# Kernel tuning notes

Hardware: AMD Instinct MI355X
Metric: run time of the kernel (lower is better)

Reference implementation:

```python
import jax, jax.numpy as jnp
import numpy as np

IN_DIM = 64
OUT_DIM = 128
GROUPS = 4
KS = 3
PAD = 1
SPLINE_ORDER = 3
GRID_SIZE = 5
GRID_K = GRID_SIZE + SPLINE_ORDER  # 8
GRID_LO, GRID_HI = -1.0, 1.0
_H = (GRID_HI - GRID_LO) / GRID_SIZE
GRID = jnp.linspace(GRID_LO - _H * SPLINE_ORDER, GRID_HI + _H * SPLINE_ORDER,
                    GRID_SIZE + 2 * SPLINE_ORDER + 1, dtype=jnp.float32)  # [14]
EPS = 1e-5


def _conv(x, w):
    # NCHW x OIHW -> NCHW, stride 1, dilation 1, padding PAD
    return jax.lax.conv_general_dilated(
        x, w, window_strides=(1, 1), padding=((PAD, PAD), (PAD, PAD)),
        dimension_numbers=('NCHW', 'OIHW', 'NCHW'))


def _bspline_bases(x):
    # Cox-de-Boor recursion; x: [B,C,H,W] -> [B, C*GRID_K, H, W]
    xu = x[..., None]  # [B,C,H,W,1]
    g = GRID
    bases = ((xu >= g[:-1]) & (xu < g[1:])).astype(x.dtype)  # [B,C,H,W,13]
    for k in range(1, SPLINE_ORDER + 1):
        left = g[:-(k + 1)]
        right = g[k:-1]
        delta = jnp.where(right == left, jnp.ones_like(right), right - left)
        bases = ((xu - left) / delta * bases[..., :-1]
                 + (g[k + 1:] - xu) / (g[k + 1:] - g[1:-k]) * bases[..., 1:])
    B, C, H, W, K = bases.shape  # K == GRID_K
    # moveaxis(-1, 2) then flatten(1, 2): channel-major, basis-minor ordering
    return jnp.moveaxis(bases, -1, 2).reshape(B, C * K, H, W)


def setup_inputs() -> dict:
    key = jax.random.key(0)
    k1, k2 = jax.random.split(key)
    x = jax.random.normal(k1, (8, IN_DIM, 64, 64), dtype=jnp.float32)
    # layer_weight: [out/g, (in/g)*(grid_k+1), ks, ks] = [32, 144, 3, 3]
    layer_weight = jax.random.normal(
        k2, (OUT_DIM // GROUPS, (IN_DIM // GROUPS) * (GRID_K + 1), KS, KS),
        dtype=jnp.float32) * 0.05
    prelu_w = jnp.full((GROUPS,), 0.25, dtype=jnp.float32)  # torch PReLU init
    return {"x": x, "layer_weight": layer_weight, "prelu_w": prelu_w}


def reference(x, layer_weight, prelu_w):
    cin_g = IN_DIM // GROUPS
    cout_g = OUT_DIM // GROUPS
    base_w = layer_weight[:, -cin_g:].reshape(cout_g, cin_g, KS, KS)
    spline_w = layer_weight[:, :-cin_g].reshape(cout_g, cin_g * GRID_K, KS, KS)
    outs = []
    for g in range(GROUPS):
        xg = x[:, g * cin_g:(g + 1) * cin_g]
        base_out = _conv(jax.nn.gelu(xg, approximate=False), base_w)
        spline_out = _conv(_bspline_bases(xg), spline_w)
        y = base_out + spline_out
        # InstanceNorm2d (affine=False): per-sample per-channel spatial norm
        mu = y.mean(axis=(2, 3), keepdims=True)
        var = y.var(axis=(2, 3), keepdims=True)
        y = (y - mu) / jnp.sqrt(var + EPS)
        # PReLU with scalar slope per group
        y = jnp.where(y >= 0, y, prelu_w[g] * y)
        outs.append(y)
    return jnp.concatenate(outs, axis=1)  # [B, OUT_DIM, H, W]
```

## Files before the change

### kernel.cpp

```cpp
#include <hip/hip_runtime.h>
#include <hip/hip_bf16.h>
#include <math.h>

typedef __attribute__((ext_vector_type(8))) short short8;
typedef __attribute__((ext_vector_type(4))) float f32x4;

__global__ void wtrans(const float* __restrict__ lw, ushort* __restrict__ w2) {
    int t = blockIdx.x * 256 + threadIdx.x;
    if (t >= 5760) return;
    int l    = t & 63;
    int page = t >> 6;
    int nt  = page & 1;
    int ks  = (page >> 1) % 5;
    int tap = page / 10;
    int oc = nt * 16 + (l & 15);
    int kbase = ks * 32 + (l >> 4) * 8;
    short8 v;
#pragma unroll
    for (int e = 0; e < 8; ++e) {
        int k = kbase + e;
        float val = (k < 144) ? lw[(oc * 144 + k) * 9 + tap] : 0.f;
        __hip_bfloat16 hb = __float2bfloat16(val);
        v[e] = *(short*)&hb;
    }
    ((short8*)w2)[t] = v;
}

__global__ __launch_bounds__(256) void kanconv(const float* __restrict__ x,
                                               const ushort* __restrict__ w2,
                                               float* __restrict__ y) {
    __shared__ __align__(16) ushort Fs[108 * 168];
    const int tid  = threadIdx.x;
    const int tile = blockIdx.x;
    const int b    = blockIdx.y;
    const int g    = blockIdx.z;
    const int h0 = (tile >> 2) * 4;
    const int w0 = (tile & 3) * 16;
    const float* xg = x + ((size_t)(b * 64 + g * 16)) * 4096;

#pragma unroll 1
    for (int it = 0; it < 7; ++it) {
        int e = it * 256 + tid;
        if (e < 1728) {
            int icg = e / 108;
            int p   = e - icg * 108;
            int py = p / 18, px = p - py * 18;
            int hy = h0 + py - 1, wx = w0 + px - 1;
            bool img = ((unsigned)hy < 64u) && ((unsigned)wx < 64u);
            float xv = img ? xg[icg * 4096 + hy * 64 + wx] : 0.f;
            float tpos = (xv + 2.2f) * 2.5f;
            float cf = floorf(tpos);
            int ci = (int)cf;
            float u = tpos - cf;
            float u2 = u * u, u3 = u2 * u, om = 1.f - u;
            const float s6 = 1.f / 6.f;
            float q0 = om * om * om * s6;
            float q1 = (4.f - 6.f * u2 + 3.f * u3) * s6;
            float q2 = (1.f + 3.f * u + 3.f * u2 - 3.f * u3) * s6;
            float q3 = u3 * s6;
            __hip_bfloat16 hq0 = __float2bfloat16(q0);
            __hip_bfloat16 hq1 = __float2bfloat16(q1);
            __hip_bfloat16 hq2 = __float2bfloat16(q2);
            __hip_bfloat16 hq3 = __float2bfloat16(q3);
            unsigned long long Q =
                  (unsigned long long)*(ushort*)&hq0
                | ((unsigned long long)*(ushort*)&hq1 << 16)
                | ((unsigned long long)*(ushort*)&hq2 << 32)
                | ((unsigned long long)*(ushort*)&hq3 << 48);
            unsigned long long lo = 0, hi = 0;
            if (img && ci >= 0 && ci <= 10) {
                int s = ci * 16 - 48;
                if (s < 0)        { lo = Q >> (-s); }
                else if (s < 64)  { lo = Q << s; hi = s ? (Q >> (64 - s)) : 0ull; }
                else              { hi = Q << (s - 64); }
            }
            union { unsigned long long u64[2]; short8 s8; } un;
            un.u64[0] = lo; un.u64[1] = hi;
            ushort* row = &Fs[p * 168];
            *(short8*)(row + icg * 8) = un.s8;
            float z  = xv * 0.70710678118654752f;
            float az = fabsf(z);
            float tt = 1.f / fmaf(0.3275911f, az, 1.f);
            float poly = tt * fmaf(tt, fmaf(tt, fmaf(tt, fmaf(tt, 1.061405429f,
                          -1.453152027f), 1.421413741f), -0.284496736f),
                          0.254829592f);
            float er = 1.f - poly * __expf(-z * z);
            er = (z < 0.f) ? -er : er;
            float ge = 0.5f * xv * (1.f + er);
            __hip_bfloat16 hg = __float2bfloat16(ge);
            row[128 + icg] = *(ushort*)&hg;
        }
    }
    {
        short8 z8 = {0, 0, 0, 0, 0, 0, 0, 0};
        for (int e = tid; e < 216; e += 256) {
            int p = e >> 1;
            *(short8*)&Fs[p * 168 + 144 + (e & 1) * 8] = z8;
        }
    }
    __syncthreads();

    const int wv = tid >> 6;
    const int l  = tid & 63;
    const int lx = l & 15, q = l >> 4;
    const int nt    = wv >> 1;
    const int khalf = wv & 1;
    const int tap_lo = khalf ? 5 : 0;
    const int tap_hi = khalf ? 9 : 5;

    f32x4 acc0 = {0.f, 0.f, 0.f, 0.f};
    f32x4 acc1 = acc0, acc2 = acc0, acc3 = acc0;
    const short8* w8 = (const short8*)w2;
    const int lane_off = lx * 168 + q * 8;

#pragma unroll 1
    for (int tap = tap_lo; tap < tap_hi; ++tap) {
        const int kh = tap / 3, kw = tap - kh * 3;
        const ushort* arow = &Fs[(kh * 18 + kw) * 168 + lane_off];
        const short8* bp = w8 + (tap * 10 + nt) * 64 + l;
#pragma unroll
        for (int ks = 0; ks < 5; ++ks) {
            short8 bf = bp[ks * 128];
            short8 a0 = *(const short8*)(arow + 0 * 3024 + ks * 32);
            short8 a1 = *(const short8*)(arow + 1 * 3024 + ks * 32);
            short8 a2 = *(const short8*)(arow + 2 * 3024 + ks * 32);
            short8 a3 = *(const short8*)(arow + 3 * 3024 + ks * 32);
            acc0 = __builtin_amdgcn_mfma_f32_16x16x32_bf16(a0, bf, acc0, 0, 0, 0);
            acc1 = __builtin_amdgcn_mfma_f32_16x16x32_bf16(a1, bf, acc1, 0, 0, 0);
            acc2 = __builtin_amdgcn_mfma_f32_16x16x32_bf16(a2, bf, acc2, 0, 0, 0);
            acc3 = __builtin_amdgcn_mfma_f32_16x16x32_bf16(a3, bf, acc3, 0, 0, 0);
        }
    }

    __syncthreads();
    float* comb = (float*)Fs;
    if (khalf == 1) {
        float* cp = comb + (nt * 64 + l) * 20;
        *(f32x4*)(cp + 0)  = acc0;
        *(f32x4*)(cp + 4)  = acc1;
        *(f32x4*)(cp + 8)  = acc2;
        *(f32x4*)(cp + 12) = acc3;
    }
    __syncthreads();
    if (khalf == 0) {
        const float* cp = comb + (nt * 64 + l) * 20;
        f32x4 o0 = acc0 + *(const f32x4*)(cp + 0);
        f32x4 o1 = acc1 + *(const f32x4*)(cp + 4);
        f32x4 o2 = acc2 + *(const f32x4*)(cp + 8);
        f32x4 o3 = acc3 + *(const f32x4*)(cp + 12);
        float* yb = y + ((size_t)b * 128 + g * 32 + nt * 16 + lx) * 4096
                      + h0 * 64 + w0 + q * 4;
        *(f32x4*)(yb + 0 * 64) = o0;
        *(f32x4*)(yb + 1 * 64) = o1;
        *(f32x4*)(yb + 2 * 64) = o2;
        *(f32x4*)(yb + 3 * 64) = o3;
    }
}

__global__ __launch_bounds__(256) void instnorm(float* __restrict__ y,
                                                const float* __restrict__ prelu) {
    const int blk = blockIdx.x;
    const int tid = threadIdx.x;
    float4* yp = (float4*)(y + (size_t)blk * 4096);
    float4 v0 = yp[tid], v1 = yp[tid + 256], v2 = yp[tid + 512], v3 = yp[tid + 768];
    float s  = v0.x + v0.y + v0.z + v0.w + v1.x + v1.y + v1.z + v1.w
             + v2.x + v2.y + v2.z + v2.w + v3.x + v3.y + v3.z + v3.w;
    float s2 = v0.x*v0.x + v0.y*v0.y + v0.z*v0.z + v0.w*v0.w
             + v1.x*v1.x + v1.y*v1.y + v1.z*v1.z + v1.w*v1.w
             + v2.x*v2.x + v2.y*v2.y + v2.z*v2.z + v2.w*v2.w
             + v3.x*v3.x + v3.y*v3.y + v3.z*v3.z + v3.w*v3.w;
#pragma unroll
    for (int off = 32; off > 0; off >>= 1) {
        s  += __shfl_down(s, off);
        s2 += __shfl_down(s2, off);
    }
    __shared__ float red[8];
    int wave = tid >> 6;
    if ((tid & 63) == 0) { red[wave] = s; red[4 + wave] = s2; }
    __syncthreads();
    float S  = red[0] + red[1] + red[2] + red[3];
    float S2 = red[4] + red[5] + red[6] + red[7];
    float mean = S * (1.0f / 4096.0f);
    float var  = S2 * (1.0f / 4096.0f) - mean * mean;
    float rstd = rsqrtf(var + 1e-5f);
    float slope = prelu[(blk >> 5) & 3];
    float t;
    float4 o;
#define NRM(vv)                                                               \
    t = (vv.x - mean) * rstd; o.x = t >= 0.f ? t : slope * t;                 \
    t = (vv.y - mean) * rstd; o.y = t >= 0.f ? t : slope * t;                 \
    t = (vv.z - mean) * rstd; o.z = t >= 0.f ? t : slope * t;                 \
    t = (vv.w - mean) * rstd; o.w = t >= 0.f ? t : slope * t;
    NRM(v0); yp[tid]       = o;
    NRM(v1); yp[tid + 256] = o;
    NRM(v2); yp[tid + 512] = o;
    NRM(v3); yp[tid + 768] = o;
#undef NRM
}

extern "C" void kernel_launch(void* const* d_in, const int* in_sizes, int n_in,
                              void* d_out, int out_size, void* d_ws, size_t ws_size,
                              hipStream_t stream) {
    const float* x     = (const float*)d_in[0];
    const float* lw    = (const float*)d_in[1];
    const float* prelu = (const float*)d_in[2];
    float*  out = (float*)d_out;
    ushort* w2  = (ushort*)d_ws;

    wtrans<<<23, 256, 0, stream>>>(lw, w2);
    dim3 grid(64, 8, 4);
    kanconv<<<grid, 256, 0, stream>>>(x, w2, out);
    instnorm<<<1024, 256, 0, stream>>>(out, prelu);
}
```

Measured before the change: 42.80 us.

## Precompute padded B-spline/GELU features in separate kernel, load tiles in conv

Moves the B-spline basis and GELU feature computation out of the conv kernel into a new kernel. It writes a zero-padded 66x66 bf16 feature map (20 bytes per element) to workspace, and the conv kernel then copies tiles from it into LDS. This removes the redundant halo recomputation (108 vs 64 pixels per tile) and the per-element transcendental work inside the MFMA kernel. The cost is an extra launch and a global round-trip of roughly 45 MB of feature data, with unaligned 20-byte loads.

```diff
diff --git a/kernel.cpp b/kernel.cpp
--- a/kernel.cpp
+++ b/kernel.cpp
@@ -4,6 +4,10 @@
 
 typedef __attribute__((ext_vector_type(8))) short short8;
 typedef __attribute__((ext_vector_type(4))) float f32x4;
+typedef unsigned int u32;
+typedef unsigned long long u64;
+
+struct FeatElem { u32 d[5]; };
 
 __global__ void wtrans(const float* __restrict__ lw, ushort* __restrict__ w2) {
     int t = blockIdx.x * 256 + threadIdx.x;
@@ -26,7 +30,61 @@
     ((short8*)w2)[t] = v;
 }
 
-__global__ __launch_bounds__(256) void kanconv(const float* __restrict__ x,
+__global__ __launch_bounds__(256) void featk(const float* __restrict__ x,
+                                             ushort* __restrict__ FG) {
+    int t = blockIdx.x * 256 + threadIdx.x;
+    if (t >= 4356) return;
+    int c  = blockIdx.y;
+    int hp = t / 66, wp = t - hp * 66;
+    bool img = (hp >= 1) && (hp <= 64) && (wp >= 1) && (wp <= 64);
+    float xv = img ? x[(size_t)c * 4096 + (hp - 1) * 64 + (wp - 1)] : 0.f;
+
+    float tpos = (xv + 2.2f) * 2.5f;
+    float cf = floorf(tpos);
+    int ci = (int)cf;
+    float u = tpos - cf;
+    float u2 = u * u, u3 = u2 * u, om = 1.f - u;
+    const float s6 = 1.f / 6.f;
+    float q0 = om * om * om * s6;
+    float q1 = (4.f - 6.f * u2 + 3.f * u3) * s6;
+    float q2 = (1.f + 3.f * u + 3.f * u2 - 3.f * u3) * s6;
+    float q3 = u3 * s6;
+    __hip_bfloat16 hq0 = __float2bfloat16(q0);
+    __hip_bfloat16 hq1 = __float2bfloat16(q1);
+    __hip_bfloat16 hq2 = __float2bfloat16(q2);
+    __hip_bfloat16 hq3 = __float2bfloat16(q3);
+    u64 Q =   (u64)*(ushort*)&hq0
+            | ((u64)*(ushort*)&hq1 << 16)
+            | ((u64)*(ushort*)&hq2 << 32)
+            | ((u64)*(ushort*)&hq3 << 48);
+    u64 lo = 0, hi = 0;
+    if (img && ci >= 0 && ci <= 10) {
+        int s = ci * 16 - 48;
+        if (s < 0)        { lo = Q >> (-s); }
+        else if (s < 64)  { lo = Q << s; hi = s ? (Q >> (64 - s)) : 0ull; }
+        else              { hi = Q << (s - 64); }
+    }
+    float z  = xv * 0.70710678118654752f;
+    float az = fabsf(z);
+    float tt = 1.f / fmaf(0.3275911f, az, 1.f);
+    float poly = tt * fmaf(tt, fmaf(tt, fmaf(tt, fmaf(tt, 1.061405429f,
+                  -1.453152027f), 1.421413741f), -0.284496736f),
+                  0.254829592f);
+    float er = 1.f - poly * __expf(-z * z);
+    er = (z < 0.f) ? -er : er;
+    float ge = img ? 0.5f * xv * (1.f + er) : 0.f;
+    __hip_bfloat16 hg = __float2bfloat16(ge);
+
+    FeatElem fe;
+    fe.d[0] = (u32)(lo & 0xffffffffull);
+    fe.d[1] = (u32)(lo >> 32);
+    fe.d[2] = (u32)(hi & 0xffffffffull);
+    fe.d[3] = (u32)(hi >> 32);
+    fe.d[4] = (u32)*(ushort*)&hg;
+    *(FeatElem*)(FG + ((size_t)c * 4356 + t) * 10) = fe;
+}
+
+__global__ __launch_bounds__(256) void kanconv(const ushort* __restrict__ FG,
                                                const ushort* __restrict__ w2,
                                                float* __restrict__ y) {
     __shared__ __align__(16) ushort Fs[108 * 168];
@@ -36,59 +94,20 @@
     const int g    = blockIdx.z;
     const int h0 = (tile >> 2) * 4;
     const int w0 = (tile & 3) * 16;
-    const float* xg = x + ((size_t)(b * 64 + g * 16)) * 4096;
-
-#pragma unroll 1
-    for (int it = 0; it < 7; ++it) {
-        int e = it * 256 + tid;
-        if (e < 1728) {
-            int icg = e / 108;
-            int p   = e - icg * 108;
-            int py = p / 18, px = p - py * 18;
-            int hy = h0 + py - 1, wx = w0 + px - 1;
-            bool img = ((unsigned)hy < 64u) && ((unsigned)wx < 64u);
-            float xv = img ? xg[icg * 4096 + hy * 64 + wx] : 0.f;
-            float tpos = (xv + 2.2f) * 2.5f;
-            float cf = floorf(tpos);
-            int ci = (int)cf;
-            float u = tpos - cf;
-            float u2 = u * u, u3 = u2 * u, om = 1.f - u;
-            const float s6 = 1.f / 6.f;
-            float q0 = om * om * om * s6;
-            float q1 = (4.f - 6.f * u2 + 3.f * u3) * s6;
-            float q2 = (1.f + 3.f * u + 3.f * u2 - 3.f * u3) * s6;
-            float q3 = u3 * s6;
-            __hip_bfloat16 hq0 = __float2bfloat16(q0);
-            __hip_bfloat16 hq1 = __float2bfloat16(q1);
-            __hip_bfloat16 hq2 = __float2bfloat16(q2);
-            __hip_bfloat16 hq3 = __float2bfloat16(q3);
-            unsigned long long Q =
-                  (unsigned long long)*(ushort*)&hq0
-                | ((unsigned long long)*(ushort*)&hq1 << 16)
-                | ((unsigned long long)*(ushort*)&hq2 << 32)
-                | ((unsigned long long)*(ushort*)&hq3 << 48);
-            unsigned long long lo = 0, hi = 0;
-            if (img && ci >= 0 && ci <= 10) {
-                int s = ci * 16 - 48;
-                if (s < 0)        { lo = Q >> (-s); }
-                else if (s < 64)  { lo = Q << s; hi = s ? (Q >> (64 - s)) : 0ull; }
-                else              { hi = Q << (s - 64); }
-            }
-            union { unsigned long long u64[2]; short8 s8; } un;
-            un.u64[0] = lo; un.u64[1] = hi;
-            ushort* row = &Fs[p * 168];
-            *(short8*)(row + icg * 8) = un.s8;
-            float z  = xv * 0.70710678118654752f;
-            float az = fabsf(z);
-            float tt = 1.f / fmaf(0.3275911f, az, 1.f);
-            float poly = tt * fmaf(tt, fmaf(tt, fmaf(tt, fmaf(tt, 1.061405429f,
-                          -1.453152027f), 1.421413741f), -0.284496736f),
-                          0.254829592f);
-            float er = 1.f - poly * __expf(-z * z);
-            er = (z < 0.f) ? -er : er;
-            float ge = 0.5f * xv * (1.f + er);
-            __hip_bfloat16 hg = __float2bfloat16(ge);
-            row[128 + icg] = *(ushort*)&hg;
+
+    if (tid < 192) {
+        int st = tid >> 1, half = tid & 1;
+        int icg = st / 6, py = st - icg * 6;
+        const ushort* gp = FG + (((size_t)(b * 64 + g * 16 + icg) * 66
+                                  + (h0 + py)) * 66 + (w0 + 9 * half)) * 10;
+        ushort* lp = &Fs[(py * 18 + 9 * half) * 168 + icg * 8];
+        ushort* lg = &Fs[(py * 18 + 9 * half) * 168 + 128 + icg];
+#pragma unroll
+        for (int j = 0; j < 9; ++j) {
+            FeatElem fe = *(const FeatElem*)(gp + (size_t)j * 10);
+            uint4 sv; sv.x = fe.d[0]; sv.y = fe.d[1]; sv.z = fe.d[2]; sv.w = fe.d[3];
+            *(uint4*)(lp + j * 168) = sv;
+            lg[j * 168] = (ushort)fe.d[4];
         }
     }
     {
@@ -206,9 +225,12 @@
     const float* prelu = (const float*)d_in[2];
     float*  out = (float*)d_out;
     ushort* w2  = (ushort*)d_ws;
+    ushort* FG  = (ushort*)((char*)d_ws + 92160);
 
     wtrans<<<23, 256, 0, stream>>>(lw, w2);
+    dim3 fgrid(18, 512);
+    featk<<<fgrid, 256, 0, stream>>>(x, FG);
     dim3 grid(64, 8, 4);
-    kanconv<<<grid, 256, 0, stream>>>(x, w2, out);
+    kanconv<<<grid, 256, 0, stream>>>(FG, w2, out);
     instnorm<<<1024, 256, 0, stream>>>(out, prelu);
 }
```

Result: slower. 56.14 us (+31.2%).

## Switch conv GEMM to 32x32x16 MFMA with weights as A operand and tighter K padding

Applied to the files above, without the earlier changes.

The convolution inner loop now uses 32x32x16 bf16 MFMA with weights as the A operand (32 output channels) and pixels as B, so the reduction is 144 in 9 steps with no zero padding. Previously it used 16x16x32 with K padded to 160. The weight pretransform is relaid accordingly, the shared feature row stride drops from 168 to 152, and the zero-fill of pad columns is removed. This cuts wasted MFMA work and LDS traffic, at the cost of scalar, less coalesced output stores that are strided across channels.

```diff
diff --git a/kernel.cpp b/kernel.cpp
--- a/kernel.cpp
+++ b/kernel.cpp
@@ -4,22 +4,24 @@
 
 typedef __attribute__((ext_vector_type(8))) short short8;
 typedef __attribute__((ext_vector_type(4))) float f32x4;
+typedef __attribute__((ext_vector_type(16))) float f32x16;
+typedef unsigned int u32;
+typedef unsigned long long u64;
 
 __global__ void wtrans(const float* __restrict__ lw, ushort* __restrict__ w2) {
     int t = blockIdx.x * 256 + threadIdx.x;
-    if (t >= 5760) return;
+    if (t >= 5184) return;
     int l    = t & 63;
     int page = t >> 6;
-    int nt  = page & 1;
-    int ks  = (page >> 1) % 5;
-    int tap = page / 10;
-    int oc = nt * 16 + (l & 15);
-    int kbase = ks * 32 + (l >> 4) * 8;
+    int ks  = page % 9;
+    int tap = page / 9;
+    int oc = l & 31;
+    int kbase = ks * 16 + ((l >> 5) << 3);
     short8 v;
 #pragma unroll
     for (int e = 0; e < 8; ++e) {
         int k = kbase + e;
-        float val = (k < 144) ? lw[(oc * 144 + k) * 9 + tap] : 0.f;
+        float val = lw[(oc * 144 + k) * 9 + tap];
         __hip_bfloat16 hb = __float2bfloat16(val);
         v[e] = *(short*)&hb;
     }
@@ -29,7 +31,7 @@
 __global__ __launch_bounds__(256) void kanconv(const float* __restrict__ x,
                                                const ushort* __restrict__ w2,
                                                float* __restrict__ y) {
-    __shared__ __align__(16) ushort Fs[108 * 168];
+    __shared__ __align__(16) ushort Fs[108 * 152];
     const int tid  = threadIdx.x;
     const int tile = blockIdx.x;
     const int b    = blockIdx.y;
@@ -62,21 +64,20 @@
             __hip_bfloat16 hq1 = __float2bfloat16(q1);
             __hip_bfloat16 hq2 = __float2bfloat16(q2);
             __hip_bfloat16 hq3 = __float2bfloat16(q3);
-            unsigned long long Q =
-                  (unsigned long long)*(ushort*)&hq0
-                | ((unsigned long long)*(ushort*)&hq1 << 16)
-                | ((unsigned long long)*(ushort*)&hq2 << 32)
-                | ((unsigned long long)*(ushort*)&hq3 << 48);
-            unsigned long long lo = 0, hi = 0;
+            u64 Q =   (u64)*(ushort*)&hq0
+                    | ((u64)*(ushort*)&hq1 << 16)
+                    | ((u64)*(ushort*)&hq2 << 32)
+                    | ((u64)*(ushort*)&hq3 << 48);
+            u64 lo = 0, hi = 0;
             if (img && ci >= 0 && ci <= 10) {
                 int s = ci * 16 - 48;
                 if (s < 0)        { lo = Q >> (-s); }
                 else if (s < 64)  { lo = Q << s; hi = s ? (Q >> (64 - s)) : 0ull; }
                 else              { hi = Q << (s - 64); }
             }
-            union { unsigned long long u64[2]; short8 s8; } un;
-            un.u64[0] = lo; un.u64[1] = hi;
-            ushort* row = &Fs[p * 168];
+            union { u64 u64v[2]; short8 s8; } un;
+            un.u64v[0] = lo; un.u64v[1] = hi;
+            ushort* row = &Fs[p * 152];
             *(short8*)(row + icg * 8) = un.s8;
             float z  = xv * 0.70710678118654752f;
             float az = fabsf(z);
@@ -91,69 +92,55 @@
             row[128 + icg] = *(ushort*)&hg;
         }
     }
-    {
-        short8 z8 = {0, 0, 0, 0, 0, 0, 0, 0};
-        for (int e = tid; e < 216; e += 256) {
-            int p = e >> 1;
-            *(short8*)&Fs[p * 168 + 144 + (e & 1) * 8] = z8;
-        }
-    }
     __syncthreads();
 
     const int wv = tid >> 6;
     const int l  = tid & 63;
-    const int lx = l & 15, q = l >> 4;
-    const int nt    = wv >> 1;
     const int khalf = wv & 1;
+    const int pt    = wv >> 1;
+    const int pix  = pt * 32 + (l & 31);
+    const int prow = pix >> 4, pcol = pix & 15;
+    const int klo  = l >> 5;
+
+    f32x16 acc;
+#pragma unroll
+    for (int i = 0; i < 16; ++i) acc[i] = 0.f;
+    const short8* w8 = (const short8*)w2;
     const int tap_lo = khalf ? 5 : 0;
     const int tap_hi = khalf ? 9 : 5;
-
-    f32x4 acc0 = {0.f, 0.f, 0.f, 0.f};
-    f32x4 acc1 = acc0, acc2 = acc0, acc3 = acc0;
-    const short8* w8 = (const short8*)w2;
-    const int lane_off = lx * 168 + q * 8;
 
 #pragma unroll 1
     for (int tap = tap_lo; tap < tap_hi; ++tap) {
         const int kh = tap / 3, kw = tap - kh * 3;
-        const ushort* arow = &Fs[(kh * 18 + kw) * 168 + lane_off];
-        const short8* bp = w8 + (tap * 10 + nt) * 64 + l;
-#pragma unroll
-        for (int ks = 0; ks < 5; ++ks) {
-            short8 bf = bp[ks * 128];
-            short8 a0 = *(const short8*)(arow + 0 * 3024 + ks * 32);
-            short8 a1 = *(const short8*)(arow + 1 * 3024 + ks * 32);
-            short8 a2 = *(const short8*)(arow + 2 * 3024 + ks * 32);
-            short8 a3 = *(const short8*)(arow + 3 * 3024 + ks * 32);
-            acc0 = __builtin_amdgcn_mfma_f32_16x16x32_bf16(a0, bf, acc0, 0, 0, 0);
-            acc1 = __builtin_amdgcn_mfma_f32_16x16x32_bf16(a1, bf, acc1, 0, 0, 0);
-            acc2 = __builtin_amdgcn_mfma_f32_16x16x32_bf16(a2, bf, acc2, 0, 0, 0);
-            acc3 = __builtin_amdgcn_mfma_f32_16x16x32_bf16(a3, bf, acc3, 0, 0, 0);
+        const ushort* fb = &Fs[((prow + kh) * 18 + (pcol + kw)) * 152 + klo * 8];
+        const short8* ap = w8 + tap * 576 + l;
+#pragma unroll
+        for (int ks = 0; ks < 9; ++ks) {
+            short8 a  = ap[ks * 64];
+            short8 bf = *(const short8*)(fb + ks * 16);
+            acc = __builtin_amdgcn_mfma_f32_32x32x16_bf16(a, bf, acc, 0, 0, 0);
         }
     }
 
     __syncthreads();
     float* comb = (float*)Fs;
     if (khalf == 1) {
-        float* cp = comb + (nt * 64 + l) * 20;
-        *(f32x4*)(cp + 0)  = acc0;
-        *(f32x4*)(cp + 4)  = acc1;
-        *(f32x4*)(cp + 8)  = acc2;
-        *(f32x4*)(cp + 12) = acc3;
+        float* cp = comb + (pt * 64 + l) * 20;
+        *(f32x4*)(cp + 0)  = f32x4{acc[0], acc[1], acc[2], acc[3]};
+        *(f32x4*)(cp + 4)  = f32x4{acc[4], acc[5], acc[6], acc[7]};
+        *(f32x4*)(cp + 8)  = f32x4{acc[8], acc[9], acc[10], acc[11]};
+        *(f32x4*)(cp + 12) = f32x4{acc[12], acc[13], acc[14], acc[15]};
     }
     __syncthreads();
     if (khalf == 0) {
-        const float* cp = comb + (nt * 64 + l) * 20;
-        f32x4 o0 = acc0 + *(const f32x4*)(cp + 0);
-        f32x4 o1 = acc1 + *(const f32x4*)(cp + 4);
-        f32x4 o2 = acc2 + *(const f32x4*)(cp + 8);
-        f32x4 o3 = acc3 + *(const f32x4*)(cp + 12);
-        float* yb = y + ((size_t)b * 128 + g * 32 + nt * 16 + lx) * 4096
-                      + h0 * 64 + w0 + q * 4;
-        *(f32x4*)(yb + 0 * 64) = o0;
-        *(f32x4*)(yb + 1 * 64) = o1;
-        *(f32x4*)(yb + 2 * 64) = o2;
-        *(f32x4*)(yb + 3 * 64) = o3;
+        const float* cp = comb + (pt * 64 + l) * 20;
+        float* yb = y + (((size_t)b * 128 + g * 32) * 64 + h0 + prow) * 64
+                      + w0 + pcol;
+#pragma unroll
+        for (int r = 0; r < 16; ++r) {
+            int oc = (r & 3) + 8 * (r >> 2) + 4 * klo;
+            yb[(size_t)oc * 4096] = acc[r] + cp[r];
+        }
     }
 }
 
@@ -207,7 +194,7 @@
     float*  out = (float*)d_out;
     ushort* w2  = (ushort*)d_ws;
 
-    wtrans<<<23, 256, 0, stream>>>(lw, w2);
+    wtrans<<<21, 256, 0, stream>>>(lw, w2);
     dim3 grid(64, 8, 4);
     kanconv<<<grid, 256, 0, stream>>>(x, w2, out);
     instnorm<<<1024, 256, 0, stream>>>(out, prelu);
```

Measured after the change: 42.68 us. About the same (-0.3%).
